# Kernel tuning notes

Hardware: AMD Instinct MI355X
Metric: run time of the kernel (lower is better)

## Reference

```python
import jax, jax.numpy as jnp
import numpy as np

C = 512
EPS = 1e-5


def _layer_norm(x, gamma, beta):
    mu = jnp.mean(x, axis=-1, keepdims=True)
    var = jnp.var(x, axis=-1, keepdims=True)
    return (x - mu) * jax.lax.rsqrt(var + EPS) * gamma + beta


def setup_inputs() -> dict:
    key = jax.random.key(0)
    ks = jax.random.split(key, 12)
    B, L = 8, 2048
    s = 1.0 / np.sqrt(C)
    return {
        "x1": jax.random.normal(ks[0], (B, C, L), dtype=jnp.float32),
        "x2": jax.random.normal(ks[1], (B, C, L), dtype=jnp.float32),
        "w_q": jax.random.normal(ks[2], (C, C), dtype=jnp.float32) * s,
        "b_q": jax.random.normal(ks[3], (C,), dtype=jnp.float32) * s,
        "w_k": jax.random.normal(ks[4], (C, C), dtype=jnp.float32) * s,
        "b_k": jax.random.normal(ks[5], (C,), dtype=jnp.float32) * s,
        "w_v1": jax.random.normal(ks[6], (C, C), dtype=jnp.float32) * s,
        "b_v1": jax.random.normal(ks[7], (C,), dtype=jnp.float32) * s,
        "w_v2": jax.random.normal(ks[8], (C, C), dtype=jnp.float32) * s,
        "b_v2": jax.random.normal(ks[9], (C,), dtype=jnp.float32) * s,
        "ln_gamma": jnp.ones((C,), dtype=jnp.float32),
        "ln_beta": jnp.zeros((C,), dtype=jnp.float32),
    }


def reference(x1, x2, w_q, b_q, w_k, b_k, w_v1, b_v1, w_v2, b_v2, ln_gamma, ln_beta):
    # (B, C, L) -> (B, L, C)
    x1 = jnp.swapaxes(x1, 1, 2)
    x2 = jnp.swapaxes(x2, 1, 2)
    # torch Linear: y = x @ W^T + b
    q = jnp.einsum("blc,dc->bld", x1, w_q) + b_q
    k = jnp.einsum("blc,dc->bld", x2, w_k) + b_k
    v1 = jnp.einsum("blc,dc->bld", x1, w_v1) + b_v1
    v2 = jnp.einsum("blc,dc->bld", x2, w_v2) + b_v2
    # shared attention scores [B, L1, L2]
    attn = jnp.einsum("bqc,bkc->bqk", q, k) / jnp.sqrt(jnp.float32(C))
    attn_k = jax.nn.softmax(attn, axis=-1)          # rows (over L2)
    attn_q = jax.nn.softmax(attn, axis=1)           # cols (over L1)
    vk = jnp.einsum("bqk,bkc->bqc", attn_k, v2)     # [B, L1, C]
    vq = jnp.einsum("bqk,bqc->bkc", attn_q, v1)     # [B, L2, C]
    # cross skip + shared layernorm
    r1 = _layer_norm(vk + x1, ln_gamma, ln_beta)
    r2 = _layer_norm(vq + x2, ln_gamma, ln_beta)
    return (jnp.swapaxes(r1, 1, 2), jnp.swapaxes(r2, 1, 2))
```

## Files before the change

kernel.cpp:

```cpp
#include <hip/hip_runtime.h>

#define L_DIM 2048
#define C_DIM 512
#define B_DIM 8

typedef __attribute__((ext_vector_type(8))) short bf16x8;
typedef __attribute__((ext_vector_type(4))) float f32x4;

constexpr size_t SQ  = (size_t)L_DIM * C_DIM;
constexpr size_t SAT = (size_t)L_DIM * L_DIM;
constexpr size_t MC  = (size_t)B_DIM * L_DIM * C_DIM;
constexpr int BL = B_DIM * L_DIM;

__device__ float g_psr[16][BL];
__device__ float g_psc[16][BL];
__device__ float g_sinv[2][BL];

__device__ __forceinline__ float bf2f(ushort u) {
  union { float f; unsigned int i; } c; c.i = ((unsigned int)u) << 16; return c.f;
}
__device__ __forceinline__ ushort f2bf(float f) {
  union { float f; unsigned int i; } c; c.f = f;
  unsigned int lsb = (c.i >> 16) & 1u;
  return (ushort)((c.i + 0x7FFFu + lsb) >> 16);
}

__device__ __forceinline__ float wave_red_sum(float v) {
  #pragma unroll
  for (int o = 1; o < 64; o <<= 1) v += __shfl_xor(v, o, 64);
  return v;
}

__device__ __forceinline__ void glds16(const ushort* g, ushort* l) {
  __builtin_amdgcn_global_load_lds(
      (const __attribute__((address_space(1))) void*)g,
      (__attribute__((address_space(3))) void*)l, 16, 0, 0);
}

__device__ __forceinline__ int slotAB(int r, int c) {
  return (((c ^ (r & 7)) + (r >> 3)) & 7);
}
__device__ __forceinline__ int chAB(int r, int sl) {
  return ((sl - (r >> 3)) & 7) ^ (r & 7);
}
__device__ __forceinline__ int slotC(int r, int q4) {
  return ((q4 ^ (r & 15)) + (r >> 4)) & 15;
}

__device__ __forceinline__ int xcd_swz(int bid, int nwg) {
  return (bid & 7) * (nwg >> 3) + (bid >> 3);
}

template <bool STATS, bool SCALE>
__device__ __forceinline__ void gemm_core128(
    const ushort* __restrict__ Ab, const ushort* __restrict__ Bb,
    const float* __restrict__ bias,
    ushort* __restrict__ obN, ushort* __restrict__ obT,
    const int K, const int lda, const int ldb, const int ldo, const int ldoT,
    const int m0, const int n0, const float scale, const int EPI,
    const int sb, const float* __restrict__ stati)
{
  __shared__ __align__(16) ushort lds[16384];
  __shared__ float sinv[128];

  const int t = threadIdx.x;
  const int lane = t & 63, w = t >> 6;
  const int wr = w >> 1, wc = w & 1;
  const int l16 = lane & 15, lhi = lane >> 4;
  const int lrow = lane >> 3, lsl = lane & 7;

  ushort* As = lds;
  ushort* Bs = lds + 8192;

  if (SCALE) {
    if (t < 128) sinv[t] = stati[t];
  }

  f32x4 acc[4][4];
  #pragma unroll
  for (int i = 0; i < 4; ++i)
    #pragma unroll
    for (int j = 0; j < 4; ++j) { f32x4 zv = {0.f, 0.f, 0.f, 0.f}; acc[i][j] = zv; }

  const int KT = K >> 6;
  for (int kt = 0; kt < KT; ++kt) {
    const int k0 = kt << 6;
    __syncthreads();
    #pragma unroll
    for (int p = 0; p < 4; ++p) {
      const int rbase = w * 32 + p * 8;
      const int rr = rbase + lrow;
      const int ch = chAB(rr, lsl);
      glds16(Ab + (size_t)(m0 + rr) * lda + k0 + ch * 8, As + rbase * 64);
      glds16(Bb + (size_t)(n0 + rr) * ldb + k0 + ch * 8, Bs + rbase * 64);
    }
    __syncthreads();
    #pragma unroll
    for (int ks = 0; ks < 2; ++ks) {
      bf16x8 af[4], bg[4];
      #pragma unroll
      for (int i = 0; i < 4; ++i) {
        const int ra = wr * 64 + i * 16 + l16;
        af[i] = *(const bf16x8*)&As[ra * 64 + 8 * slotAB(ra, ks * 4 + lhi)];
        const int rb = wc * 64 + i * 16 + l16;
        bg[i] = *(const bf16x8*)&Bs[rb * 64 + 8 * slotAB(rb, ks * 4 + lhi)];
      }
      #pragma unroll
      for (int i = 0; i < 4; ++i)
        #pragma unroll
        for (int j = 0; j < 4; ++j)
          acc[i][j] = __builtin_amdgcn_mfma_f32_16x16x32_bf16(af[i], bg[j], acc[i][j], 0, 0, 0);
    }
  }

  __syncthreads();
  ushort* Cs = lds;
  #pragma unroll
  for (int i = 0; i < 4; ++i) {
    #pragma unroll
    for (int j = 0; j < 4; ++j) {
      const int er = wr * 64 + i * 16 + lhi * 4;
      const int ec = wc * 64 + j * 16 + l16;
      const float bv = bias ? bias[n0 + ec] : 0.f;
      #pragma unroll
      for (int r = 0; r < 4; ++r) {
        const int rr = er + r;
        float val = acc[i][j][r] * scale + bv;
        if (STATS) val = __expf(val);
        if (SCALE) val *= sinv[rr];
        Cs[rr * 128 + 8 * slotC(rr, ec >> 3) + (ec & 7)] = f2bf(val);
      }
    }
  }
  __syncthreads();
  if (EPI == 0 || EPI == 2) {
    #pragma unroll
    for (int p = 0; p < 8; ++p) {
      const int id = p * 256 + t, r = id >> 4, cc = id & 15;
      const bf16x8 v = *(const bf16x8*)&Cs[r * 128 + 8 * slotC(r, cc)];
      *(bf16x8*)(obN + (size_t)(m0 + r) * ldo + n0 + cc * 8) = v;
    }
  }
  if (EPI >= 1) {
    #pragma unroll
    for (int p = 0; p < 8; ++p) {
      const int id = p * 256 + t, c = id >> 4, rs = id & 15;
      bf16x8 tv;
      #pragma unroll
      for (int jj = 0; jj < 8; ++jj) {
        const int r2 = rs * 8 + jj;
        tv[jj] = (short)Cs[r2 * 128 + 8 * slotC(r2, c >> 3) + (c & 7)];
      }
      *(bf16x8*)(obT + (size_t)(n0 + c) * ldoT + m0 + rs * 8) = tv;
    }
  }

  if (STATS) {
    if (t < 128) {
      const int r = t;
      float s = 0.f;
      #pragma unroll
      for (int cc = 0; cc < 16; ++cc) {
        const bf16x8 v8 = *(const bf16x8*)&Cs[r * 128 + 8 * slotC(r, cc)];
        #pragma unroll
        for (int j = 0; j < 8; ++j) s += bf2f((ushort)v8[j]);
      }
      g_psr[n0 >> 7][sb * L_DIM + m0 + r] = s;
    } else {
      const int c = t - 128;
      float s = 0.f;
      #pragma unroll 8
      for (int r2 = 0; r2 < 128; ++r2)
        s += bf2f(Cs[r2 * 128 + 8 * slotC(r2, c >> 3) + (c & 7)]);
      g_psc[m0 >> 7][sb * L_DIM + n0 + c] = s;
    }
  }
}

__global__ __launch_bounds__(256, 4) void gemm_proj(
    const ushort* __restrict__ x1T, const ushort* __restrict__ x2T,
    const ushort* __restrict__ wbf,
    const float* __restrict__ b_q, const float* __restrict__ b_k,
    const float* __restrict__ b_v1, const float* __restrict__ b_v2,
    ushort* __restrict__ q, ushort* __restrict__ kb,
    ushort* __restrict__ v1T, ushort* __restrict__ v2T)
{
  const int lid = xcd_swz(blockIdx.x, 2048);
  const int x = lid & 15, y = (lid >> 4) & 3, rest = lid >> 6;
  const int b = rest & 7, pj = rest >> 3;
  const ushort* A = ((pj & 1) ? x2T : x1T) + (size_t)b * SQ;
  const ushort* B = wbf + (size_t)pj * (C_DIM * C_DIM);
  const float* bias = pj == 0 ? b_q : pj == 1 ? b_k : pj == 2 ? b_v1 : b_v2;
  if (pj < 2) {
    ushort* oN = (pj == 0 ? q : kb) + (size_t)b * SQ;
    gemm_core128<false, false>(A, B, bias, oN, nullptr, C_DIM, C_DIM, C_DIM,
                               C_DIM, 0, x * 128, y * 128, 1.0f, 0, 0, nullptr);
  } else {
    ushort* oT = (pj == 2 ? v1T : v2T) + (size_t)b * SQ;
    gemm_core128<false, false>(A, B, bias, nullptr, oT, C_DIM, C_DIM, C_DIM,
                               0, L_DIM, x * 128, y * 128, 1.0f, 1, 0, nullptr);
  }
}

__global__ __launch_bounds__(256, 4) void gemm_qkt(
    const ushort* __restrict__ qb, const ushort* __restrict__ kb,
    ushort* __restrict__ attn, ushort* __restrict__ attnT, const float scale)
{
  const int lid = xcd_swz(blockIdx.x, 2048);
  const int x = lid & 15, y = (lid >> 4) & 15, b = lid >> 8;
  gemm_core128<true, false>(qb + (size_t)b * SQ, kb + (size_t)b * SQ, nullptr,
               attn + (size_t)b * SAT, attnT + (size_t)b * SAT,
               C_DIM, C_DIM, C_DIM, L_DIM, L_DIM,
               x * 128, y * 128, scale, 2, b, nullptr);
}

__global__ __launch_bounds__(256) void sm_combine()
{
  const int i = blockIdx.x * 256 + threadIdx.x;
  const int which = blockIdx.y;
  const float* ps = which ? &g_psc[0][0] : &g_psr[0][0];
  float s = 0.f;
  #pragma unroll
  for (int p = 0; p < 16; ++p) s += ps[p * BL + i];
  g_sinv[which][i] = 1.0f / s;
}

__global__ __launch_bounds__(256, 4) void gemm_pv(
    const ushort* __restrict__ attn, const ushort* __restrict__ attnT,
    const ushort* __restrict__ v1T, const ushort* __restrict__ v2T,
    ushort* __restrict__ vk, ushort* __restrict__ vq)
{
  const int lid = xcd_swz(blockIdx.x, 1024);
  const int x = lid & 15, y = (lid >> 4) & 3, rest = lid >> 6;
  const int which = rest & 1, b = rest >> 1;
  const ushort* A = (which ? attnT : attn) + (size_t)b * SAT;
  const ushort* B = (which ? v1T : v2T) + (size_t)b * SQ;
  ushort* o = (which ? vq : vk) + (size_t)b * SQ;
  const int m0 = x * 128;
  gemm_core128<false, true>(A, B, nullptr, o, nullptr,
               L_DIM, L_DIM, L_DIM, C_DIM, 0,
               m0, y * 128, 1.0f, 0, b, &g_sinv[which][b * L_DIM + m0]);
}

__global__ __launch_bounds__(256) void xpose(const float* __restrict__ x1,
                                             const float* __restrict__ x2,
                                             ushort* __restrict__ xT)
{
  __shared__ float s[64][65];
  const int z = blockIdx.z, l0 = blockIdx.x * 64, c0 = blockIdx.y * 64;
  const int t = threadIdx.x;
  const float* xb = (z < 8 ? x1 : x2) + ((size_t)(z & 7) * C_DIM + c0) * L_DIM + l0;
  #pragma unroll
  for (int p = 0; p < 16; ++p) {
    const int c = p * 4 + (t >> 6);
    s[c][t & 63] = xb[(size_t)c * L_DIM + (t & 63)];
  }
  __syncthreads();
  ushort* ob = xT + (size_t)z * SQ + (size_t)l0 * C_DIM + c0;
  #pragma unroll
  for (int p = 0; p < 16; ++p) {
    const int l = p * 4 + (t >> 6);
    ob[(size_t)l * C_DIM + (t & 63)] = f2bf(s[t & 63][l]);
  }
}

__global__ __launch_bounds__(256) void cvtw4(const float* __restrict__ a,
    const float* __restrict__ b, const float* __restrict__ c,
    const float* __restrict__ d, ushort* __restrict__ o)
{
  const int i = blockIdx.x * 256 + threadIdx.x;
  const int sel = i >> 18;
  const float* w = sel == 0 ? a : sel == 1 ? b : sel == 2 ? c : d;
  o[i] = f2bf(w[i & 262143]);
}

__global__ __launch_bounds__(256) void ln_out(const ushort* __restrict__ vk,
    const ushort* __restrict__ vq, const float* __restrict__ x1,
    const float* __restrict__ x2, const float* __restrict__ gamma,
    const float* __restrict__ beta, float* __restrict__ out)
{
  __shared__ float s[16][513];
  __shared__ float mu[16], rsd[16];
  __shared__ float gb[512], bb[512];
  const int t = threadIdx.x;
  const int b = blockIdx.y, l0 = blockIdx.x * 16, which = blockIdx.z;
  const ushort* vx = which ? vq : vk;
  const float* xo = which ? x2 : x1;
  float* obase = out + (size_t)which * MC;
  #pragma unroll
  for (int r = 0; r < 2; ++r) { gb[r * 256 + t] = gamma[r * 256 + t]; bb[r * 256 + t] = beta[r * 256 + t]; }
  const ushort* vb = vx + ((size_t)b * L_DIM + l0) * C_DIM;
  #pragma unroll
  for (int p = 0; p < 4; ++p) {
    const int id = p * 256 + t;
    const int l = id >> 6, cb = (id & 63) * 8;
    bf16x8 v = *(const bf16x8*)&vb[(size_t)l * C_DIM + cb];
    #pragma unroll
    for (int j = 0; j < 8; ++j) s[l][cb + j] = bf2f((ushort)v[j]);
  }
  __syncthreads();
  const float* xb = xo + (size_t)b * C_DIM * L_DIM + l0;
  for (int it = 0; it < 32; ++it) {
    const int idx = it * 256 + t, c = idx >> 4, l = idx & 15;
    s[l][c] += xb[(size_t)c * L_DIM + l];
  }
  __syncthreads();
  const int w = t >> 6, lane = t & 63;
  #pragma unroll
  for (int rr = 0; rr < 4; ++rr) {
    const int l = w * 4 + rr;
    float sum = 0.f, sq = 0.f;
    #pragma unroll
    for (int c0 = 0; c0 < 512; c0 += 64) {
      const float v = s[l][c0 + lane];
      sum += v; sq = fmaf(v, v, sq);
    }
    sum = wave_red_sum(sum); sq = wave_red_sum(sq);
    if (lane == 0) {
      const float m = sum * (1.f / 512.f);
      const float var = sq * (1.f / 512.f) - m * m;
      mu[l] = m; rsd[l] = rsqrtf(var + 1e-5f);
    }
  }
  __syncthreads();
  float* ob = obase + (size_t)b * C_DIM * L_DIM + l0;
  for (int it = 0; it < 32; ++it) {
    const int idx = it * 256 + t, c = idx >> 4, l = idx & 15;
    const float v = (s[l][c] - mu[l]) * rsd[l] * gb[c] + bb[c];
    ob[(size_t)c * L_DIM + l] = v;
  }
}

extern "C" void kernel_launch(void* const* d_in, const int* in_sizes, int n_in,
                              void* d_out, int out_size, void* d_ws, size_t ws_size,
                              hipStream_t stream) {
  const float* x1   = (const float*)d_in[0];
  const float* x2   = (const float*)d_in[1];
  const float* w_q  = (const float*)d_in[2];
  const float* b_q  = (const float*)d_in[3];
  const float* w_k  = (const float*)d_in[4];
  const float* b_k  = (const float*)d_in[5];
  const float* w_v1 = (const float*)d_in[6];
  const float* b_v1 = (const float*)d_in[7];
  const float* w_v2 = (const float*)d_in[8];
  const float* b_v2 = (const float*)d_in[9];
  const float* gamma= (const float*)d_in[10];
  const float* beta = (const float*)d_in[11];
  float* out = (float*)d_out;

  ushort* q    = (ushort*)d_ws;
  ushort* kbuf = q + MC;
  ushort* v1T  = kbuf + MC;
  ushort* v2T  = v1T + MC;
  ushort* attn = v2T + MC;
  ushort* x1T = attn;
  ushort* wbf = attn + 2 * MC;
  ushort* vkbuf = kbuf;
  ushort* vqbuf = q;
  ushort* attnT = (ushort*)d_out;

  const float iscale = 0.044194173824159216f;
  const dim3 blk256(256);

  cvtw4<<<4096, blk256, 0, stream>>>(w_q, w_k, w_v1, w_v2, wbf);
  xpose<<<dim3(32, 8, 16), blk256, 0, stream>>>(x1, x2, x1T);
  gemm_proj<<<2048, blk256, 0, stream>>>(x1T, x1T + MC, wbf,
      b_q, b_k, b_v1, b_v2, q, kbuf, v1T, v2T);
  gemm_qkt<<<2048, blk256, 0, stream>>>(q, kbuf, attn, attnT, iscale);
  sm_combine<<<dim3(BL / 256, 2), blk256, 0, stream>>>();
  gemm_pv<<<1024, blk256, 0, stream>>>(attn, attnT, v1T, v2T, vkbuf, vqbuf);
  ln_out<<<dim3(L_DIM / 16, B_DIM, 2), blk256, 0, stream>>>(
      vkbuf, vqbuf, x1, x2, gamma, beta, out);
}
```

Measured before the change: 263.3 us.

## Triple-buffer GEMM K-loop with async LDS loads and fold softmax combine into PV

The shared GEMM core now keeps three LDS stages and issues global-to-LDS loads two tiles ahead, waiting with explicit vmcnt and a single barrier per iteration instead of two syncthreads. The goal is to overlap memory latency with MFMA work. The separate sm_combine kernel is removed, and each PV block now sums the 16 partial softmax denominators itself when it loads its 128 inverse scales, saving a launch. LDS use rises to 96KB per block and launch bounds drop to one block per SIMD group, which lowers occupancy and adds redundant partial-sum reads across the N tiles.

```diff
diff --git a/kernel.cpp b/kernel.cpp
--- a/kernel.cpp
+++ b/kernel.cpp
@@ -14,7 +14,6 @@
 
 __device__ float g_psr[16][BL];
 __device__ float g_psc[16][BL];
-__device__ float g_sinv[2][BL];
 
 __device__ __forceinline__ float bf2f(ushort u) {
   union { float f; unsigned int i; } c; c.i = ((unsigned int)u) << 16; return c.f;
@@ -58,9 +57,9 @@
     ushort* __restrict__ obN, ushort* __restrict__ obT,
     const int K, const int lda, const int ldb, const int ldo, const int ldoT,
     const int m0, const int n0, const float scale, const int EPI,
-    const int sb, const float* __restrict__ stati)
-{
-  __shared__ __align__(16) ushort lds[16384];
+    const int sb, const float* __restrict__ ps)
+{
+  __shared__ __align__(16) ushort lds[49152];
   __shared__ float sinv[128];
 
   const int t = threadIdx.x;
@@ -69,11 +68,13 @@
   const int l16 = lane & 15, lhi = lane >> 4;
   const int lrow = lane >> 3, lsl = lane & 7;
 
-  ushort* As = lds;
-  ushort* Bs = lds + 8192;
-
   if (SCALE) {
-    if (t < 128) sinv[t] = stati[t];
+    if (t < 128) {
+      float s = 0.f;
+      #pragma unroll
+      for (int p = 0; p < 16; ++p) s += ps[(size_t)p * BL + t];
+      sinv[t] = 1.0f / s;
+    }
   }
 
   f32x4 acc[4][4];
@@ -82,19 +83,32 @@
     #pragma unroll
     for (int j = 0; j < 4; ++j) { f32x4 zv = {0.f, 0.f, 0.f, 0.f}; acc[i][j] = zv; }
 
-  const int KT = K >> 6;
-  for (int kt = 0; kt < KT; ++kt) {
-    const int k0 = kt << 6;
-    __syncthreads();
+  auto stage = [&](ushort* base, int k0) {
     #pragma unroll
     for (int p = 0; p < 4; ++p) {
       const int rbase = w * 32 + p * 8;
       const int rr = rbase + lrow;
       const int ch = chAB(rr, lsl);
-      glds16(Ab + (size_t)(m0 + rr) * lda + k0 + ch * 8, As + rbase * 64);
-      glds16(Bb + (size_t)(n0 + rr) * ldb + k0 + ch * 8, Bs + rbase * 64);
-    }
-    __syncthreads();
+      glds16(Ab + (size_t)(m0 + rr) * lda + k0 + ch * 8, base + rbase * 64);
+      glds16(Bb + (size_t)(n0 + rr) * ldb + k0 + ch * 8, base + 8192 + rbase * 64);
+    }
+  };
+
+  const int KT = K >> 6;
+  ushort* cur = lds;
+  ushort* nxt = lds + 16384;
+  ushort* fut = lds + 32768;
+  stage(cur, 0);
+  stage(nxt, 64);
+  __builtin_amdgcn_sched_barrier(0);
+  asm volatile("s_waitcnt vmcnt(8) lgkmcnt(0)" ::: "memory");
+  __builtin_amdgcn_s_barrier();
+  __builtin_amdgcn_sched_barrier(0);
+
+  for (int kt = 0; kt < KT; ++kt) {
+    if (kt + 2 < KT) stage(fut, (kt + 2) << 6);
+    const ushort* As = cur;
+    const ushort* Bs = cur + 8192;
     #pragma unroll
     for (int ks = 0; ks < 2; ++ks) {
       bf16x8 af[4], bg[4];
@@ -111,9 +125,14 @@
         for (int j = 0; j < 4; ++j)
           acc[i][j] = __builtin_amdgcn_mfma_f32_16x16x32_bf16(af[i], bg[j], acc[i][j], 0, 0, 0);
     }
-  }
-
-  __syncthreads();
+    __builtin_amdgcn_sched_barrier(0);
+    if (kt + 2 < KT)      asm volatile("s_waitcnt vmcnt(8)" ::: "memory");
+    else if (kt + 1 < KT) asm volatile("s_waitcnt vmcnt(0)" ::: "memory");
+    __builtin_amdgcn_s_barrier();
+    __builtin_amdgcn_sched_barrier(0);
+    ushort* tmp = cur; cur = nxt; nxt = fut; fut = tmp;
+  }
+
   ushort* Cs = lds;
   #pragma unroll
   for (int i = 0; i < 4; ++i) {
@@ -177,7 +196,7 @@
   }
 }
 
-__global__ __launch_bounds__(256, 4) void gemm_proj(
+__global__ __launch_bounds__(256, 1) void gemm_proj(
     const ushort* __restrict__ x1T, const ushort* __restrict__ x2T,
     const ushort* __restrict__ wbf,
     const float* __restrict__ b_q, const float* __restrict__ b_k,
@@ -202,7 +221,7 @@
   }
 }
 
-__global__ __launch_bounds__(256, 4) void gemm_qkt(
+__global__ __launch_bounds__(256, 1) void gemm_qkt(
     const ushort* __restrict__ qb, const ushort* __restrict__ kb,
     ushort* __restrict__ attn, ushort* __restrict__ attnT, const float scale)
 {
@@ -214,18 +233,7 @@
                x * 128, y * 128, scale, 2, b, nullptr);
 }
 
-__global__ __launch_bounds__(256) void sm_combine()
-{
-  const int i = blockIdx.x * 256 + threadIdx.x;
-  const int which = blockIdx.y;
-  const float* ps = which ? &g_psc[0][0] : &g_psr[0][0];
-  float s = 0.f;
-  #pragma unroll
-  for (int p = 0; p < 16; ++p) s += ps[p * BL + i];
-  g_sinv[which][i] = 1.0f / s;
-}
-
-__global__ __launch_bounds__(256, 4) void gemm_pv(
+__global__ __launch_bounds__(256, 1) void gemm_pv(
     const ushort* __restrict__ attn, const ushort* __restrict__ attnT,
     const ushort* __restrict__ v1T, const ushort* __restrict__ v2T,
     ushort* __restrict__ vk, ushort* __restrict__ vq)
@@ -237,9 +245,10 @@
   const ushort* B = (which ? v1T : v2T) + (size_t)b * SQ;
   ushort* o = (which ? vq : vk) + (size_t)b * SQ;
   const int m0 = x * 128;
+  const float* ps = (which ? &g_psc[0][0] : &g_psr[0][0]) + b * L_DIM + m0;
   gemm_core128<false, true>(A, B, nullptr, o, nullptr,
                L_DIM, L_DIM, L_DIM, C_DIM, 0,
-               m0, y * 128, 1.0f, 0, b, &g_sinv[which][b * L_DIM + m0]);
+               m0, y * 128, 1.0f, 0, b, ps);
 }
 
 __global__ __launch_bounds__(256) void xpose(const float* __restrict__ x1,
@@ -367,7 +376,6 @@
   gemm_proj<<<2048, blk256, 0, stream>>>(x1T, x1T + MC, wbf,
       b_q, b_k, b_v1, b_v2, q, kbuf, v1T, v2T);
   gemm_qkt<<<2048, blk256, 0, stream>>>(q, kbuf, attn, attnT, iscale);
-  sm_combine<<<dim3(BL / 256, 2), blk256, 0, stream>>>();
   gemm_pv<<<1024, blk256, 0, stream>>>(attn, attnT, v1T, v2T, vkbuf, vqbuf);
   ln_out<<<dim3(L_DIM / 16, B_DIM, 2), blk256, 0, stream>>>(
       vkbuf, vqbuf, x1, x2, gamma, beta, out);
```

After: 406.1 us. +54.2%, slower.

## Enlarge GEMM tiles to 256x128 and fold softmax sum combine into PV GEMM

Applied to the files above, without the earlier changes.

Each GEMM block now computes a 256x128 output tile with 8x4 MFMA accumulators per wave, halving grid sizes and reusing each B fragment across more A rows. The epilogue runs in two 128-row halves through the same LDS staging buffer. The separate sm_combine kernel is removed: the PV GEMM sums the partial softmax denominators itself and takes the reciprocal, and the column partials now use 8 slots instead of 16. The aim is more data reuse and one fewer launch, at the cost of more registers, lower occupancy (launch bounds 2) and fewer blocks to fill the device.

```diff
diff --git a/kernel.cpp b/kernel.cpp
--- a/kernel.cpp
+++ b/kernel.cpp
@@ -13,8 +13,7 @@
 constexpr int BL = B_DIM * L_DIM;
 
 __device__ float g_psr[16][BL];
-__device__ float g_psc[16][BL];
-__device__ float g_sinv[2][BL];
+__device__ float g_psc[8][BL];
 
 __device__ __forceinline__ float bf2f(ushort u) {
   union { float f; unsigned int i; } c; c.i = ((unsigned int)u) << 16; return c.f;
@@ -52,16 +51,16 @@
 }
 
 template <bool STATS, bool SCALE>
-__device__ __forceinline__ void gemm_core128(
+__device__ __forceinline__ void gemm_core(
     const ushort* __restrict__ Ab, const ushort* __restrict__ Bb,
     const float* __restrict__ bias,
     ushort* __restrict__ obN, ushort* __restrict__ obT,
     const int K, const int lda, const int ldb, const int ldo, const int ldoT,
     const int m0, const int n0, const float scale, const int EPI,
-    const int sb, const float* __restrict__ stati)
-{
-  __shared__ __align__(16) ushort lds[16384];
-  __shared__ float sinv[128];
+    const int sb, const float* __restrict__ ps, const int npart)
+{
+  __shared__ __align__(16) ushort lds[24576];
+  __shared__ float sinv[256];
 
   const int t = threadIdx.x;
   const int lane = t & 63, w = t >> 6;
@@ -70,15 +69,17 @@
   const int lrow = lane >> 3, lsl = lane & 7;
 
   ushort* As = lds;
-  ushort* Bs = lds + 8192;
+  ushort* Bs = lds + 16384;
 
   if (SCALE) {
-    if (t < 128) sinv[t] = stati[t];
-  }
-
-  f32x4 acc[4][4];
-  #pragma unroll
-  for (int i = 0; i < 4; ++i)
+    float s = 0.f;
+    for (int p = 0; p < npart; ++p) s += ps[(size_t)p * BL + t];
+    sinv[t] = 1.0f / s;
+  }
+
+  f32x4 acc[8][4];
+  #pragma unroll
+  for (int i = 0; i < 8; ++i)
     #pragma unroll
     for (int j = 0; j < 4; ++j) { f32x4 zv = {0.f, 0.f, 0.f, 0.f}; acc[i][j] = zv; }
 
@@ -87,97 +88,113 @@
     const int k0 = kt << 6;
     __syncthreads();
     #pragma unroll
+    for (int p = 0; p < 8; ++p) {
+      const int rbase = w * 64 + p * 8;
+      const int rr = rbase + lrow;
+      const int ch = chAB(rr, lsl);
+      glds16(Ab + (size_t)(m0 + rr) * lda + k0 + ch * 8, As + rbase * 64);
+    }
+    #pragma unroll
     for (int p = 0; p < 4; ++p) {
       const int rbase = w * 32 + p * 8;
       const int rr = rbase + lrow;
       const int ch = chAB(rr, lsl);
-      glds16(Ab + (size_t)(m0 + rr) * lda + k0 + ch * 8, As + rbase * 64);
       glds16(Bb + (size_t)(n0 + rr) * ldb + k0 + ch * 8, Bs + rbase * 64);
     }
     __syncthreads();
     #pragma unroll
     for (int ks = 0; ks < 2; ++ks) {
-      bf16x8 af[4], bg[4];
-      #pragma unroll
-      for (int i = 0; i < 4; ++i) {
-        const int ra = wr * 64 + i * 16 + l16;
-        af[i] = *(const bf16x8*)&As[ra * 64 + 8 * slotAB(ra, ks * 4 + lhi)];
-        const int rb = wc * 64 + i * 16 + l16;
-        bg[i] = *(const bf16x8*)&Bs[rb * 64 + 8 * slotAB(rb, ks * 4 + lhi)];
-      }
-      #pragma unroll
-      for (int i = 0; i < 4; ++i)
+      bf16x8 bg[4];
+      #pragma unroll
+      for (int j = 0; j < 4; ++j) {
+        const int rb = wc * 64 + j * 16 + l16;
+        bg[j] = *(const bf16x8*)&Bs[rb * 64 + 8 * slotAB(rb, ks * 4 + lhi)];
+      }
+      #pragma unroll
+      for (int i = 0; i < 8; ++i) {
+        const int ra = wr * 128 + i * 16 + l16;
+        const bf16x8 af = *(const bf16x8*)&As[ra * 64 + 8 * slotAB(ra, ks * 4 + lhi)];
         #pragma unroll
         for (int j = 0; j < 4; ++j)
-          acc[i][j] = __builtin_amdgcn_mfma_f32_16x16x32_bf16(af[i], bg[j], acc[i][j], 0, 0, 0);
+          acc[i][j] = __builtin_amdgcn_mfma_f32_16x16x32_bf16(af, bg[j], acc[i][j], 0, 0, 0);
+      }
     }
   }
 
   __syncthreads();
   ushort* Cs = lds;
-  #pragma unroll
-  for (int i = 0; i < 4; ++i) {
-    #pragma unroll
-    for (int j = 0; j < 4; ++j) {
-      const int er = wr * 64 + i * 16 + lhi * 4;
-      const int ec = wc * 64 + j * 16 + l16;
-      const float bv = bias ? bias[n0 + ec] : 0.f;
-      #pragma unroll
-      for (int r = 0; r < 4; ++r) {
-        const int rr = er + r;
-        float val = acc[i][j][r] * scale + bv;
-        if (STATS) val = __expf(val);
-        if (SCALE) val *= sinv[rr];
-        Cs[rr * 128 + 8 * slotC(rr, ec >> 3) + (ec & 7)] = f2bf(val);
-      }
-    }
-  }
-  __syncthreads();
-  if (EPI == 0 || EPI == 2) {
-    #pragma unroll
-    for (int p = 0; p < 8; ++p) {
-      const int id = p * 256 + t, r = id >> 4, cc = id & 15;
-      const bf16x8 v = *(const bf16x8*)&Cs[r * 128 + 8 * slotC(r, cc)];
-      *(bf16x8*)(obN + (size_t)(m0 + r) * ldo + n0 + cc * 8) = v;
-    }
-  }
-  if (EPI >= 1) {
-    #pragma unroll
-    for (int p = 0; p < 8; ++p) {
-      const int id = p * 256 + t, c = id >> 4, rs = id & 15;
-      bf16x8 tv;
-      #pragma unroll
-      for (int jj = 0; jj < 8; ++jj) {
-        const int r2 = rs * 8 + jj;
-        tv[jj] = (short)Cs[r2 * 128 + 8 * slotC(r2, c >> 3) + (c & 7)];
-      }
-      *(bf16x8*)(obT + (size_t)(n0 + c) * ldoT + m0 + rs * 8) = tv;
-    }
-  }
-
-  if (STATS) {
-    if (t < 128) {
-      const int r = t;
-      float s = 0.f;
-      #pragma unroll
-      for (int cc = 0; cc < 16; ++cc) {
-        const bf16x8 v8 = *(const bf16x8*)&Cs[r * 128 + 8 * slotC(r, cc)];
+  float scol = 0.f;
+  for (int h = 0; h < 2; ++h) {
+    if (h) __syncthreads();
+    if (wr == h) {
+      #pragma unroll
+      for (int i = 0; i < 4; ++i) {
+      }
+      #pragma unroll
+      for (int i = 0; i < 8; ++i) {
         #pragma unroll
-        for (int j = 0; j < 8; ++j) s += bf2f((ushort)v8[j]);
-      }
-      g_psr[n0 >> 7][sb * L_DIM + m0 + r] = s;
-    } else {
-      const int c = t - 128;
-      float s = 0.f;
-      #pragma unroll 8
-      for (int r2 = 0; r2 < 128; ++r2)
-        s += bf2f(Cs[r2 * 128 + 8 * slotC(r2, c >> 3) + (c & 7)]);
-      g_psc[m0 >> 7][sb * L_DIM + n0 + c] = s;
-    }
-  }
-}
-
-__global__ __launch_bounds__(256, 4) void gemm_proj(
+        for (int j = 0; j < 4; ++j) {
+          const int ec = wc * 64 + j * 16 + l16;
+          const float bv = bias ? bias[n0 + ec] : 0.f;
+          #pragma unroll
+          for (int r = 0; r < 4; ++r) {
+            const int rl = i * 16 + lhi * 4 + r;
+            float val = acc[i][j][r] * scale + bv;
+            if (STATS) val = __expf(val);
+            if (SCALE) val *= sinv[h * 128 + rl];
+            Cs[rl * 128 + 8 * slotC(rl, ec >> 3) + (ec & 7)] = f2bf(val);
+          }
+        }
+      }
+    }
+    __syncthreads();
+    if (EPI == 0 || EPI == 2) {
+      #pragma unroll
+      for (int p = 0; p < 8; ++p) {
+        const int id = p * 256 + t, r = id >> 4, cc = id & 15;
+        const bf16x8 v = *(const bf16x8*)&Cs[r * 128 + 8 * slotC(r, cc)];
+        *(bf16x8*)(obN + (size_t)(m0 + h * 128 + r) * ldo + n0 + cc * 8) = v;
+      }
+    }
+    if (EPI >= 1) {
+      #pragma unroll
+      for (int p = 0; p < 8; ++p) {
+        const int id = p * 256 + t, c = id >> 4, rs = id & 15;
+        bf16x8 tv;
+        #pragma unroll
+        for (int jj = 0; jj < 8; ++jj) {
+          const int r2 = rs * 8 + jj;
+          tv[jj] = (short)Cs[r2 * 128 + 8 * slotC(r2, c >> 3) + (c & 7)];
+        }
+        *(bf16x8*)(obT + (size_t)(n0 + c) * ldoT + m0 + h * 128 + rs * 8) = tv;
+      }
+    }
+    if (STATS) {
+      if (t < 128) {
+        const int r = t;
+        float s = 0.f;
+        #pragma unroll
+        for (int cc = 0; cc < 16; ++cc) {
+          const bf16x8 v8 = *(const bf16x8*)&Cs[r * 128 + 8 * slotC(r, cc)];
+          #pragma unroll
+          for (int j = 0; j < 8; ++j) s += bf2f((ushort)v8[j]);
+        }
+        g_psr[n0 >> 7][sb * L_DIM + m0 + h * 128 + r] = s;
+      } else {
+        const int c = t - 128;
+        #pragma unroll 8
+        for (int r2 = 0; r2 < 128; ++r2)
+          scol += bf2f(Cs[r2 * 128 + 8 * slotC(r2, c >> 3) + (c & 7)]);
+      }
+    }
+  }
+  if (STATS && t >= 128) {
+    const int c = t - 128;
+    g_psc[m0 >> 8][sb * L_DIM + n0 + c] = scol;
+  }
+}
+
+__global__ __launch_bounds__(256, 2) void gemm_proj(
     const ushort* __restrict__ x1T, const ushort* __restrict__ x2T,
     const ushort* __restrict__ wbf,
     const float* __restrict__ b_q, const float* __restrict__ b_k,
@@ -185,61 +202,51 @@
     ushort* __restrict__ q, ushort* __restrict__ kb,
     ushort* __restrict__ v1T, ushort* __restrict__ v2T)
 {
-  const int lid = xcd_swz(blockIdx.x, 2048);
-  const int x = lid & 15, y = (lid >> 4) & 3, rest = lid >> 6;
+  const int lid = xcd_swz(blockIdx.x, 1024);
+  const int x = lid & 7, y = (lid >> 3) & 3, rest = lid >> 5;
   const int b = rest & 7, pj = rest >> 3;
   const ushort* A = ((pj & 1) ? x2T : x1T) + (size_t)b * SQ;
   const ushort* B = wbf + (size_t)pj * (C_DIM * C_DIM);
   const float* bias = pj == 0 ? b_q : pj == 1 ? b_k : pj == 2 ? b_v1 : b_v2;
   if (pj < 2) {
     ushort* oN = (pj == 0 ? q : kb) + (size_t)b * SQ;
-    gemm_core128<false, false>(A, B, bias, oN, nullptr, C_DIM, C_DIM, C_DIM,
-                               C_DIM, 0, x * 128, y * 128, 1.0f, 0, 0, nullptr);
+    gemm_core<false, false>(A, B, bias, oN, nullptr, C_DIM, C_DIM, C_DIM,
+                            C_DIM, 0, x * 256, y * 128, 1.0f, 0, 0, nullptr, 0);
   } else {
     ushort* oT = (pj == 2 ? v1T : v2T) + (size_t)b * SQ;
-    gemm_core128<false, false>(A, B, bias, nullptr, oT, C_DIM, C_DIM, C_DIM,
-                               0, L_DIM, x * 128, y * 128, 1.0f, 1, 0, nullptr);
-  }
-}
-
-__global__ __launch_bounds__(256, 4) void gemm_qkt(
+    gemm_core<false, false>(A, B, bias, nullptr, oT, C_DIM, C_DIM, C_DIM,
+                            0, L_DIM, x * 256, y * 128, 1.0f, 1, 0, nullptr, 0);
+  }
+}
+
+__global__ __launch_bounds__(256, 2) void gemm_qkt(
     const ushort* __restrict__ qb, const ushort* __restrict__ kb,
     ushort* __restrict__ attn, ushort* __restrict__ attnT, const float scale)
 {
-  const int lid = xcd_swz(blockIdx.x, 2048);
-  const int x = lid & 15, y = (lid >> 4) & 15, b = lid >> 8;
-  gemm_core128<true, false>(qb + (size_t)b * SQ, kb + (size_t)b * SQ, nullptr,
+  const int lid = xcd_swz(blockIdx.x, 1024);
+  const int x = lid & 7, y = (lid >> 3) & 15, b = lid >> 7;
+  gemm_core<true, false>(qb + (size_t)b * SQ, kb + (size_t)b * SQ, nullptr,
                attn + (size_t)b * SAT, attnT + (size_t)b * SAT,
                C_DIM, C_DIM, C_DIM, L_DIM, L_DIM,
-               x * 128, y * 128, scale, 2, b, nullptr);
-}
-
-__global__ __launch_bounds__(256) void sm_combine()
-{
-  const int i = blockIdx.x * 256 + threadIdx.x;
-  const int which = blockIdx.y;
-  const float* ps = which ? &g_psc[0][0] : &g_psr[0][0];
-  float s = 0.f;
-  #pragma unroll
-  for (int p = 0; p < 16; ++p) s += ps[p * BL + i];
-  g_sinv[which][i] = 1.0f / s;
-}
-
-__global__ __launch_bounds__(256, 4) void gemm_pv(
+               x * 256, y * 128, scale, 2, b, nullptr, 0);
+}
+
+__global__ __launch_bounds__(256, 2) void gemm_pv(
     const ushort* __restrict__ attn, const ushort* __restrict__ attnT,
     const ushort* __restrict__ v1T, const ushort* __restrict__ v2T,
     ushort* __restrict__ vk, ushort* __restrict__ vq)
 {
-  const int lid = xcd_swz(blockIdx.x, 1024);
-  const int x = lid & 15, y = (lid >> 4) & 3, rest = lid >> 6;
+  const int lid = xcd_swz(blockIdx.x, 512);
+  const int x = lid & 7, y = (lid >> 3) & 3, rest = lid >> 5;
   const int which = rest & 1, b = rest >> 1;
   const ushort* A = (which ? attnT : attn) + (size_t)b * SAT;
   const ushort* B = (which ? v1T : v2T) + (size_t)b * SQ;
   ushort* o = (which ? vq : vk) + (size_t)b * SQ;
-  const int m0 = x * 128;
-  gemm_core128<false, true>(A, B, nullptr, o, nullptr,
+  const int m0 = x * 256;
+  const float* ps = (which ? &g_psc[0][0] : &g_psr[0][0]) + b * L_DIM + m0;
+  gemm_core<false, true>(A, B, nullptr, o, nullptr,
                L_DIM, L_DIM, L_DIM, C_DIM, 0,
-               m0, y * 128, 1.0f, 0, b, &g_sinv[which][b * L_DIM + m0]);
+               m0, y * 128, 1.0f, 0, b, ps, which ? 8 : 16);
 }
 
 __global__ __launch_bounds__(256) void xpose(const float* __restrict__ x1,
@@ -364,11 +371,10 @@
 
   cvtw4<<<4096, blk256, 0, stream>>>(w_q, w_k, w_v1, w_v2, wbf);
   xpose<<<dim3(32, 8, 16), blk256, 0, stream>>>(x1, x2, x1T);
-  gemm_proj<<<2048, blk256, 0, stream>>>(x1T, x1T + MC, wbf,
+  gemm_proj<<<1024, blk256, 0, stream>>>(x1T, x1T + MC, wbf,
       b_q, b_k, b_v1, b_v2, q, kbuf, v1T, v2T);
-  gemm_qkt<<<2048, blk256, 0, stream>>>(q, kbuf, attn, attnT, iscale);
-  sm_combine<<<dim3(BL / 256, 2), blk256, 0, stream>>>();
-  gemm_pv<<<1024, blk256, 0, stream>>>(attn, attnT, v1T, v2T, vkbuf, vqbuf);
+  gemm_qkt<<<1024, blk256, 0, stream>>>(q, kbuf, attn, attnT, iscale);
+  gemm_pv<<<512, blk256, 0, stream>>>(attn, attnT, v1T, v2T, vkbuf, vqbuf);
   ln_out<<<dim3(L_DIM / 16, B_DIM, 2), blk256, 0, stream>>>(
       vkbuf, vqbuf, x1, x2, gamma, beta, out);
 }
```

New measurement: 537.5 us. 2.04x slower.

## Fold softmax partial-sum combine into PV GEMM and widen LayerNorm tiles

Applied to the files above, without the earlier changes.

Removes the separate sm_combine kernel. Each gemm_pv block now sums the 16 softmax partial sums and takes their reciprocal for its own 128 rows, which saves a launch and a global round-trip at the cost of redundant reductions across the column-tile blocks. The ln_out kernel now handles 32 rows per block and keeps the row tile in shared memory as bf16 instead of fp32. This widens the coalesced strided reads and writes of x and out, but the residual sum is rounded to bf16 before the LayerNorm statistics, which lowers precision.

```diff
diff --git a/kernel.cpp b/kernel.cpp
--- a/kernel.cpp
+++ b/kernel.cpp
@@ -14,7 +14,6 @@
 
 __device__ float g_psr[16][BL];
 __device__ float g_psc[16][BL];
-__device__ float g_sinv[2][BL];
 
 __device__ __forceinline__ float bf2f(ushort u) {
   union { float f; unsigned int i; } c; c.i = ((unsigned int)u) << 16; return c.f;
@@ -58,7 +57,7 @@
     ushort* __restrict__ obN, ushort* __restrict__ obT,
     const int K, const int lda, const int ldb, const int ldo, const int ldoT,
     const int m0, const int n0, const float scale, const int EPI,
-    const int sb, const float* __restrict__ stati)
+    const int sb, const float* __restrict__ ps)
 {
   __shared__ __align__(16) ushort lds[16384];
   __shared__ float sinv[128];
@@ -73,7 +72,12 @@
   ushort* Bs = lds + 8192;
 
   if (SCALE) {
-    if (t < 128) sinv[t] = stati[t];
+    if (t < 128) {
+      float s = 0.f;
+      #pragma unroll
+      for (int p = 0; p < 16; ++p) s += ps[(size_t)p * BL + t];
+      sinv[t] = 1.0f / s;
+    }
   }
 
   f32x4 acc[4][4];
@@ -214,17 +218,6 @@
                x * 128, y * 128, scale, 2, b, nullptr);
 }
 
-__global__ __launch_bounds__(256) void sm_combine()
-{
-  const int i = blockIdx.x * 256 + threadIdx.x;
-  const int which = blockIdx.y;
-  const float* ps = which ? &g_psc[0][0] : &g_psr[0][0];
-  float s = 0.f;
-  #pragma unroll
-  for (int p = 0; p < 16; ++p) s += ps[p * BL + i];
-  g_sinv[which][i] = 1.0f / s;
-}
-
 __global__ __launch_bounds__(256, 4) void gemm_pv(
     const ushort* __restrict__ attn, const ushort* __restrict__ attnT,
     const ushort* __restrict__ v1T, const ushort* __restrict__ v2T,
@@ -237,9 +230,10 @@
   const ushort* B = (which ? v1T : v2T) + (size_t)b * SQ;
   ushort* o = (which ? vq : vk) + (size_t)b * SQ;
   const int m0 = x * 128;
+  const float* ps = (which ? &g_psc[0][0] : &g_psr[0][0]) + b * L_DIM + m0;
   gemm_core128<false, true>(A, B, nullptr, o, nullptr,
                L_DIM, L_DIM, L_DIM, C_DIM, 0,
-               m0, y * 128, 1.0f, 0, b, &g_sinv[which][b * L_DIM + m0]);
+               m0, y * 128, 1.0f, 0, b, ps);
 }
 
 __global__ __launch_bounds__(256) void xpose(const float* __restrict__ x1,
@@ -279,11 +273,11 @@
     const float* __restrict__ x2, const float* __restrict__ gamma,
     const float* __restrict__ beta, float* __restrict__ out)
 {
-  __shared__ float s[16][513];
-  __shared__ float mu[16], rsd[16];
+  __shared__ __align__(16) ushort s[32][520];
+  __shared__ float mu[32], rsd[32];
   __shared__ float gb[512], bb[512];
   const int t = threadIdx.x;
-  const int b = blockIdx.y, l0 = blockIdx.x * 16, which = blockIdx.z;
+  const int b = blockIdx.y, l0 = blockIdx.x * 32, which = blockIdx.z;
   const ushort* vx = which ? vq : vk;
   const float* xo = which ? x2 : x1;
   float* obase = out + (size_t)which * MC;
@@ -291,28 +285,27 @@
   for (int r = 0; r < 2; ++r) { gb[r * 256 + t] = gamma[r * 256 + t]; bb[r * 256 + t] = beta[r * 256 + t]; }
   const ushort* vb = vx + ((size_t)b * L_DIM + l0) * C_DIM;
   #pragma unroll
-  for (int p = 0; p < 4; ++p) {
+  for (int p = 0; p < 8; ++p) {
     const int id = p * 256 + t;
     const int l = id >> 6, cb = (id & 63) * 8;
-    bf16x8 v = *(const bf16x8*)&vb[(size_t)l * C_DIM + cb];
-    #pragma unroll
-    for (int j = 0; j < 8; ++j) s[l][cb + j] = bf2f((ushort)v[j]);
+    *(bf16x8*)&s[l][cb] = *(const bf16x8*)&vb[(size_t)l * C_DIM + cb];
   }
   __syncthreads();
   const float* xb = xo + (size_t)b * C_DIM * L_DIM + l0;
-  for (int it = 0; it < 32; ++it) {
-    const int idx = it * 256 + t, c = idx >> 4, l = idx & 15;
-    s[l][c] += xb[(size_t)c * L_DIM + l];
+  for (int it = 0; it < 64; ++it) {
+    const int idx = it * 256 + t, c = idx >> 5, l = idx & 31;
+    s[l][c] = f2bf(bf2f(s[l][c]) + xb[(size_t)c * L_DIM + l]);
   }
   __syncthreads();
   const int w = t >> 6, lane = t & 63;
   #pragma unroll
-  for (int rr = 0; rr < 4; ++rr) {
-    const int l = w * 4 + rr;
+  for (int rr = 0; rr < 8; ++rr) {
+    const int l = w * 8 + rr;
+    const bf16x8 v8 = *(const bf16x8*)&s[l][lane * 8];
     float sum = 0.f, sq = 0.f;
     #pragma unroll
-    for (int c0 = 0; c0 < 512; c0 += 64) {
-      const float v = s[l][c0 + lane];
+    for (int j = 0; j < 8; ++j) {
+      const float v = bf2f((ushort)v8[j]);
       sum += v; sq = fmaf(v, v, sq);
     }
     sum = wave_red_sum(sum); sq = wave_red_sum(sq);
@@ -324,9 +317,9 @@
   }
   __syncthreads();
   float* ob = obase + (size_t)b * C_DIM * L_DIM + l0;
-  for (int it = 0; it < 32; ++it) {
-    const int idx = it * 256 + t, c = idx >> 4, l = idx & 15;
-    const float v = (s[l][c] - mu[l]) * rsd[l] * gb[c] + bb[c];
+  for (int it = 0; it < 64; ++it) {
+    const int idx = it * 256 + t, c = idx >> 5, l = idx & 31;
+    const float v = (bf2f(s[l][c]) - mu[l]) * rsd[l] * gb[c] + bb[c];
     ob[(size_t)c * L_DIM + l] = v;
   }
 }
@@ -367,8 +360,7 @@
   gemm_proj<<<2048, blk256, 0, stream>>>(x1T, x1T + MC, wbf,
       b_q, b_k, b_v1, b_v2, q, kbuf, v1T, v2T);
   gemm_qkt<<<2048, blk256, 0, stream>>>(q, kbuf, attn, attnT, iscale);
-  sm_combine<<<dim3(BL / 256, 2), blk256, 0, stream>>>();
   gemm_pv<<<1024, blk256, 0, stream>>>(attn, attnT, v1T, v2T, vkbuf, vqbuf);
-  ln_out<<<dim3(L_DIM / 16, B_DIM, 2), blk256, 0, stream>>>(
+  ln_out<<<dim3(L_DIM / 32, B_DIM, 2), blk256, 0, stream>>>(
       vkbuf, vqbuf, x1, x2, gamma, beta, out);
 }
```

Result: faster. 239.7 us (median of 2 runs) (-8.9%).
